# Optimization experiments

Hardware: AMD Instinct MI355X
Metric: run time of the kernel (lower is better)

The kernel has to match this reference:

```python
import jax, jax.numpy as jnp
import numpy as np

N = 50000      # nodes
E = 800000     # edges
P = 3          # pos_dim
F = 64         # feats_dim
M = 32         # m_dim
L = 2          # n_layers
EIN = 2 * F + 1  # edge_input_dim = 129
EPS = 1e-8


def _xavier(key, shape):
    # per-layer stacked xavier-normal weights, shape = (in, out)
    fan_in, fan_out = shape
    std = (2.0 / (fan_in + fan_out)) ** 0.5
    return std * jax.random.normal(key, (L,) + shape, jnp.float32)


def setup_inputs() -> dict:
    key = jax.random.key(0)
    ks = jax.random.split(key, 10)
    x = jax.random.normal(ks[0], (N, P + F), jnp.float32)
    edge_index = jax.random.randint(ks[1], (2, E), 0, N)
    return {
        "x": x,
        "edge_index": edge_index,
        # edge_mlp: Linear(EIN, 2*EIN) -> SiLU -> Linear(2*EIN, M) -> SiLU
        "eW1": _xavier(ks[2], (EIN, 2 * EIN)), "eb1": jnp.zeros((L, 2 * EIN), jnp.float32),
        "eW2": _xavier(ks[3], (2 * EIN, M)),   "eb2": jnp.zeros((L, M), jnp.float32),
        # coors_mlp: Linear(M, 4*M) -> SiLU -> Linear(4*M, 1) -> Tanh
        "cW1": _xavier(ks[4], (M, 4 * M)),     "cb1": jnp.zeros((L, 4 * M), jnp.float32),
        "cW2": _xavier(ks[5], (4 * M, 1)),     "cb2": jnp.zeros((L, 1), jnp.float32),
        # node_mlp: Linear(F+M, 2*F) -> SiLU -> Linear(2*F, F)
        "nW1": _xavier(ks[6], (F + M, 2 * F)), "nb1": jnp.zeros((L, 2 * F), jnp.float32),
        "nW2": _xavier(ks[7], (2 * F, F)),     "nb2": jnp.zeros((L, F), jnp.float32),
        # CoorsNorm learned scale (init 0.01) per layer
        "cscale": jnp.full((L, 1), 0.01, jnp.float32),
    }


def reference(x, edge_index, eW1, eb1, eW2, eb2, cW1, cb1, cW2, cb2,
              nW1, nb1, nW2, nb2, cscale):
    src = edge_index[0]  # x_j (source)
    dst = edge_index[1]  # x_i (target / aggregation index)
    for l in range(L):
        coors, feats = x[:, :P], x[:, P:]
        rel = coors[src] - coors[dst]                       # (E, 3)
        rel_dist = jnp.sum(rel * rel, axis=-1, keepdims=True)  # (E, 1)
        # per-edge message MLP
        e_in = jnp.concatenate([feats[dst], feats[src], rel_dist], axis=-1)  # (E, 129)
        h = jax.nn.silu(e_in @ eW1[l] + eb1[l])             # (E, 258)
        m_ij = jax.nn.silu(h @ eW2[l] + eb2[l])             # (E, 32)
        # coordinate weights: SiLU MLP -> tanh
        cw = jnp.tanh(jax.nn.silu(m_ij @ cW1[l] + cb1[l]) @ cW2[l] + cb2[l])  # (E, 1)
        # CoorsNorm on rel_coors
        norm = jnp.linalg.norm(rel, axis=-1, keepdims=True)
        rel_n = rel / jnp.maximum(norm, EPS) * cscale[l]
        # scatter-aggregate (aggr='add')
        mhat_i = jax.ops.segment_sum(cw * rel_n, dst, num_segments=N)  # (N, 3)
        coors_out = coors + mhat_i
        m_i = jax.ops.segment_sum(m_ij, dst, num_segments=N)           # (N, 32)
        # node update MLP with residual
        n_in = jnp.concatenate([feats, m_i], axis=-1)                  # (N, 96)
        upd = jax.nn.silu(n_in @ nW1[l] + nb1[l]) @ nW2[l] + nb2[l]    # (N, 64)
        x = jnp.concatenate([coors_out, feats + upd], axis=-1)
    return x
```

## Files before the change

kernel.cpp:

```cpp
#include <hip/hip_runtime.h>

#define N_NODES 50000
#define N_EDGES 800000
#define PDIM 3
#define FDIM 64
#define MDIM 32
#define NLAYERS 2
#define EINDIM 129
#define H1 258
#define CH 128
#define NH 128
#define XDIM 67
#define H1T 288
#define HSTR3 104
#define W1T_K 136
#define MLSTR 40
#define NINS 104
#define NH1S 136
#define NW2K 128

typedef __attribute__((ext_vector_type(8))) short short8;
typedef __attribute__((ext_vector_type(4))) float f32x4;

#define LOG2E 1.4426950408889634f

__device__ __forceinline__ float fsilu(float x) {
  float e = __builtin_amdgcn_exp2f(-x * LOG2E);
  return x * __builtin_amdgcn_rcpf(1.0f + e);
}

__device__ __forceinline__ float ftanh(float x) {
  float xc = fminf(fmaxf(x, -15.0f), 15.0f);
  float E = __builtin_amdgcn_exp2f(2.0f * LOG2E * xc);
  return (E - 1.0f) * __builtin_amdgcn_rcpf(E + 1.0f);
}

__device__ __forceinline__ unsigned short f2bf(float f) {
  union { float f; unsigned u; } v; v.f = f;
  unsigned r = v.u + 0x7FFF + ((v.u >> 16) & 1);
  return (unsigned short)(r >> 16);
}

__device__ __forceinline__ unsigned cvt_pk(float lo, float hi) {
  unsigned r;
  asm("v_cvt_pk_bf16_f32 %0, %1, %2" : "=v"(r) : "v"(lo), "v"(hi));
  return r;
}

__device__ __forceinline__ int xcd_swz(int bid, int nwg) {
  const int nx = 8;
  int q = nwg / nx, r = nwg % nx;
  int xcd = bid % nx, idx = bid / nx;
  return (xcd < r) ? xcd * (q + 1) + idx : r * (q + 1) + (xcd - r) * q + idx;
}

#define COUNT_BLOCKS 3125
#define PREP_TOTAL (NLAYERS * (H1T * W1T_K + MDIM * H1T + CH * MDIM + 2 * H1T \
                               + NH * NINS + FDIM * NW2K))
#define PREP_BLOCKS ((PREP_TOTAL + 255) / 256)
#define CONV_BLOCKS ((N_NODES * 8 + 255) / 256)

__global__ void setup_kernel(const int* __restrict__ ei, int* __restrict__ cnt,
                             const float* __restrict__ eW1, const float* __restrict__ eW2,
                             const float* __restrict__ cW1, const float* __restrict__ eb1,
                             const float* __restrict__ nW1, const float* __restrict__ nW2,
                             unsigned short* __restrict__ w1t, unsigned short* __restrict__ w2t,
                             unsigned short* __restrict__ cw1t,
                             unsigned short* __restrict__ nw1t, unsigned short* __restrict__ nw2t,
                             float* __restrict__ b1p, float* __restrict__ wrp,
                             const float* __restrict__ X, unsigned short* __restrict__ Xb) {
  const int bid = blockIdx.x;
  const int tid = threadIdx.x;
  if (bid < COUNT_BLOCKS) {
    int e = bid * 256 + tid;
    if (e < N_EDGES) atomicAdd(&cnt[ei[N_EDGES + e]], 1);
    return;
  }
  if (bid < COUNT_BLOCKS + PREP_BLOCKS) {
    int idx = (bid - COUNT_BLOCKS) * 256 + tid;
    const int n1 = NLAYERS * H1T * W1T_K;
    const int n2 = NLAYERS * MDIM * H1T;
    const int n3 = NLAYERS * CH * MDIM;
    const int n4 = NLAYERS * H1T;
    const int n5 = NLAYERS * NH * NINS;
    const int n6 = NLAYERS * FDIM * NW2K;
    if (idx < n1) {
      int k = idx % W1T_K;
      int rest = idx / W1T_K;
      int j = rest % H1T;
      int l = rest / H1T;
      float v = (k < 128 && j < H1) ? eW1[(l * EINDIM + k) * H1 + j] : 0.0f;
      w1t[idx] = f2bf(v);
    } else if (idx < n1 + n2) {
      int t = idx - n1;
      int k = t % H1T;
      int rest = t / H1T;
      int n = rest % MDIM;
      int l = rest / MDIM;
      float v = (k < H1) ? eW2[(l * H1 + k) * MDIM + n] : 0.0f;
      w2t[t] = f2bf(v);
    } else if (idx < n1 + n2 + n3) {
      int t = idx - n1 - n2;
      int k = t % MDIM;
      int rest = t / MDIM;
      int n = rest % CH;
      int l = rest / CH;
      cw1t[t] = f2bf(cW1[(l * MDIM + k) * CH + n]);
    } else if (idx < n1 + n2 + n3 + n4) {
      int t = idx - n1 - n2 - n3;
      int j = t % H1T;
      int l = t / H1T;
      b1p[t] = (j < H1) ? eb1[l * H1 + j] : 0.0f;
    } else if (idx < n1 + n2 + n3 + 2 * n4) {
      int t = idx - n1 - n2 - n3 - n4;
      int j = t % H1T;
      int l = t / H1T;
      wrp[t] = (j < H1) ? eW1[((size_t)l * EINDIM + 128) * H1 + j] : 0.0f;
    } else if (idx < n1 + n2 + n3 + 2 * n4 + n5) {
      int t = idx - n1 - n2 - n3 - 2 * n4;
      int k = t % NINS;
      int rest = t / NINS;
      int j = rest % NH;
      int l = rest / NH;
      float v = (k < FDIM + MDIM) ? nW1[(l * (FDIM + MDIM) + k) * NH + j] : 0.0f;
      nw1t[t] = f2bf(v);
    } else if (idx < n1 + n2 + n3 + 2 * n4 + n5 + n6) {
      int t = idx - n1 - n2 - n3 - 2 * n4 - n5;
      int k = t % NW2K;
      int rest = t / NW2K;
      int j = rest % FDIM;
      int l = rest / FDIM;
      nw2t[t] = f2bf(nW2[(l * NH + k) * FDIM + j]);
    }
    return;
  }
  {
    int idx = (bid - COUNT_BLOCKS - PREP_BLOCKS) * 256 + tid;
    if (idx >= N_NODES * 8) return;
    int n = idx >> 3, c = idx & 7;
    const float* src = X + n * XDIM + PDIM + c * 8;
    short8 v;
    #pragma unroll
    for (int i = 0; i < 8; ++i) v[i] = (short)f2bf(src[i]);
    *(short8*)&Xb[n * 64 + c * 8] = v;
  }
}

__global__ __launch_bounds__(1024)
void scan_kernel(const int* __restrict__ cnt, int* __restrict__ csr, int* __restrict__ cursor) {
  __shared__ int partial[1024];
  const int tid = threadIdx.x;
  const int CHUNK = 49;
  int base = tid * CHUNK;
  int s = 0;
  for (int i = 0; i < CHUNK; ++i) {
    int idx = base + i;
    if (idx < N_NODES) s += cnt[idx];
  }
  partial[tid] = s;
  __syncthreads();
  for (int off = 1; off < 1024; off <<= 1) {
    int v = (tid >= off) ? partial[tid - off] : 0;
    __syncthreads();
    partial[tid] += v;
    __syncthreads();
  }
  int run = partial[tid] - s;
  for (int i = 0; i < CHUNK; ++i) {
    int idx = base + i;
    if (idx < N_NODES) {
      csr[idx] = run;
      cursor[idx] = run;
      run += cnt[idx];
    }
  }
  if (tid == 1023) csr[N_NODES] = run;
}

__global__ void rank_kernel(const int* __restrict__ ei, int* __restrict__ cursor,
                            int* __restrict__ srcS, int* __restrict__ dstS) {
  int e = blockIdx.x * 256 + threadIdx.x;
  if (e < N_EDGES) {
    int s = ei[e];
    int d = ei[N_EDGES + e];
    int p = atomicAdd(&cursor[d], 1);
    srcS[p] = s;
    dstS[p] = d;
  }
}

__global__ __launch_bounds__(256, 4)
void edge_mfma_kernel(const float* __restrict__ X,
                      const unsigned short* __restrict__ Xb,
                      const int* __restrict__ srcS, const int* __restrict__ dstS,
                      const unsigned short* __restrict__ w1t,
                      const float* __restrict__ b1p, const float* __restrict__ wrp,
                      const unsigned short* __restrict__ w2t, const float* __restrict__ eb2,
                      const unsigned short* __restrict__ cw1t, const float* __restrict__ cb1,
                      const float* __restrict__ cW2, const float* __restrict__ cb2,
                      const float* __restrict__ cscale,
                      unsigned short* __restrict__ ms, float* __restrict__ mh4,
                      int layer)
{
  __shared__ unsigned short hLds[128 * HSTR3];
  __shared__ unsigned short ml[128 * MLSTR];

  const int tid = threadIdx.x;
  const int lane = tid & 63;
  const int wid = tid >> 6;
  const int ln15 = lane & 15;
  const int kg = lane >> 4;
  const int e0 = xcd_swz(blockIdx.x, gridDim.x) * 128;
  const int ew0 = e0 + wid * 32;

  const int eA = ew0 + ln15;
  const int eB = ew0 + 16 + ln15;
  const int sA = srcS[eA], dA = dstS[eA];
  const int sB = srcS[eB], dB = dstS[eB];
  float rxA = X[sA * XDIM + 0] - X[dA * XDIM + 0];
  float ryA = X[sA * XDIM + 1] - X[dA * XDIM + 1];
  float rzA = X[sA * XDIM + 2] - X[dA * XDIM + 2];
  float rxB = X[sB * XDIM + 0] - X[dB * XDIM + 0];
  float ryB = X[sB * XDIM + 1] - X[dB * XDIM + 1];
  float rzB = X[sB * XDIM + 2] - X[dB * XDIM + 2];
  const float distA = rxA * rxA + ryA * ryA + rzA * rzA;
  const float distB = rxB * rxB + ryB * ryB + rzB * rzB;

  short8 einB[2][4];
  #pragma unroll
  for (int ks = 0; ks < 4; ++ks) {
    int nA = (ks < 2) ? dA : sA;
    int nB = (ks < 2) ? dB : sB;
    einB[0][ks] = *(const short8*)&Xb[nA * 64 + (ks & 1) * 32 + kg * 8];
    einB[1][ks] = *(const short8*)&Xb[nB * 64 + (ks & 1) * 32 + kg * 8];
  }

  const unsigned short* W1T = w1t + layer * H1T * W1T_K;
  const float* B1P = b1p + layer * H1T;
  const float* WRP = wrp + layer * H1T;
  const unsigned short* W2T = w2t + layer * MDIM * H1T;
  const float* B2 = eb2 + layer * MDIM;

  float b20 = B2[ln15], b21 = B2[16 + ln15];
  f32x4 mac[2][2];
  #pragma unroll
  for (int et = 0; et < 2; ++et) {
    mac[et][0] = (f32x4){b20, b20, b20, b20};
    mac[et][1] = (f32x4){b21, b21, b21, b21};
  }

  #pragma unroll 1
  for (int chunk = 0; chunk < 3; ++chunk) {
    const int jt0 = chunk * 6;
    #pragma unroll 2
    for (int jl = 0; jl < 6; ++jl) {
      const int jt = jt0 + jl;
      f32x4 b4 = *(const f32x4*)&B1P[jt * 16 + kg * 4];
      f32x4 w4 = *(const f32x4*)&WRP[jt * 16 + kg * 4];
      short8 a[4];
      #pragma unroll
      for (int ks = 0; ks < 4; ++ks)
        a[ks] = *(const short8*)&W1T[(jt * 16 + ln15) * W1T_K + ks * 32 + kg * 8];
      #pragma unroll
      for (int et = 0; et < 2; ++et) {
        const float dv = et ? distB : distA;
        f32x4 acc;
        #pragma unroll
        for (int r = 0; r < 4; ++r) acc[r] = fmaf(dv, w4[r], b4[r]);
        #pragma unroll
        for (int ks = 0; ks < 4; ++ks)
          acc = __builtin_amdgcn_mfma_f32_16x16x32_bf16(a[ks], einB[et][ks], acc, 0, 0, 0);
        uint2 uu;
        uu.x = cvt_pk(fsilu(acc[0]), fsilu(acc[1]));
        uu.y = cvt_pk(fsilu(acc[2]), fsilu(acc[3]));
        *(uint2*)&hLds[(wid * 32 + et * 16 + ln15) * HSTR3 + jl * 16 + kg * 4] = uu;
      }
    }
    #pragma unroll
    for (int ksl = 0; ksl < 3; ++ksl) {
      const int kglob = chunk * 96 + ksl * 32;
      short8 w0 = *(const short8*)&W2T[ln15 * H1T + kglob + kg * 8];
      short8 w1 = *(const short8*)&W2T[(16 + ln15) * H1T + kglob + kg * 8];
      #pragma unroll
      for (int et = 0; et < 2; ++et) {
        short8 ah = *(const short8*)&hLds[(wid * 32 + et * 16 + ln15) * HSTR3 + ksl * 32 + kg * 8];
        mac[et][0] = __builtin_amdgcn_mfma_f32_16x16x32_bf16(ah, w0, mac[et][0], 0, 0, 0);
        mac[et][1] = __builtin_amdgcn_mfma_f32_16x16x32_bf16(ah, w1, mac[et][1], 0, 0, 0);
      }
    }
  }

  #pragma unroll
  for (int et = 0; et < 2; ++et) {
    #pragma unroll
    for (int r = 0; r < 4; ++r) {
      int eg = wid * 32 + et * 16 + kg * 4 + r;
      ml[eg * MLSTR + ln15] = f2bf(fsilu(mac[et][0][r]));
      ml[eg * MLSTR + 16 + ln15] = f2bf(fsilu(mac[et][1][r]));
    }
  }

  const unsigned short* CW1T = cw1t + layer * CH * MDIM;
  const float* CB1 = cb1 + layer * CH;
  const float* CW2v = cW2 + layer * CH;
  short8 amA = *(const short8*)&ml[(wid * 32 + ln15) * MLSTR + kg * 8];
  short8 amB = *(const short8*)&ml[(wid * 32 + 16 + ln15) * MLSTR + kg * 8];
  float psA[4] = {0.f, 0.f, 0.f, 0.f};
  float psB[4] = {0.f, 0.f, 0.f, 0.f};
  #pragma unroll
  for (int nt = 0; nt < 8; ++nt) {
    float cb = CB1[nt * 16 + ln15];
    float w2v = CW2v[nt * 16 + ln15];
    short8 bc = *(const short8*)&CW1T[(nt * 16 + ln15) * MDIM + kg * 8];
    f32x4 cA = {cb, cb, cb, cb};
    f32x4 cB = {cb, cb, cb, cb};
    cA = __builtin_amdgcn_mfma_f32_16x16x32_bf16(amA, bc, cA, 0, 0, 0);
    cB = __builtin_amdgcn_mfma_f32_16x16x32_bf16(amB, bc, cB, 0, 0, 0);
    #pragma unroll
    for (int r = 0; r < 4; ++r) {
      psA[r] += fsilu(cA[r]) * w2v;
      psB[r] += fsilu(cB[r]) * w2v;
    }
  }
  #pragma unroll
  for (int off = 1; off < 16; off <<= 1) {
    #pragma unroll
    for (int r = 0; r < 4; ++r) {
      psA[r] += __shfl_xor(psA[r], off, 64);
      psB[r] += __shfl_xor(psB[r], off, 64);
    }
  }
  float cwvA = 0.0f, cwvB = 0.0f;
  #pragma unroll
  for (int r = 0; r < 4; ++r) {
    float tA = __shfl(psA[r], ((lane & 15) >> 2) * 16, 64);
    float tB = __shfl(psB[r], ((lane & 15) >> 2) * 16, 64);
    if ((lane & 3) == r) { cwvA = tA; cwvB = tB; }
  }

  #pragma unroll
  for (int it = 0; it < 2; ++it) {
    int idx = lane + it * 64;
    int el = idx >> 2, seg = idx & 3;
    short8 v = *(const short8*)&ml[(wid * 32 + el) * MLSTR + seg * 8];
    *(short8*)&ms[(size_t)(ew0 + el) * MDIM + seg * 8] = v;
  }
  if (lane < 32) {
    const int hi = lane >> 4;
    float cwv = hi ? cwvB : cwvA;
    float dv = hi ? distB : distA;
    float rx = hi ? rxB : rxA, ry = hi ? ryB : ryA, rz = hi ? rzB : rzA;
    float cw = ftanh(cwv + cb2[layer]);
    float fac = cw * cscale[layer] / fmaxf(sqrtf(dv), 1e-8f);
    *(float4*)&mh4[(size_t)(ew0 + lane) * 4] = make_float4(fac * rx, fac * ry, fac * rz, 0.0f);
  }
}

__global__ __launch_bounds__(256, 5)
void node_mfma_kernel(const float* __restrict__ Xin,
                      const unsigned short* __restrict__ XbIn,
                      const unsigned short* __restrict__ ms,
                      const float* __restrict__ mh4,
                      const int* __restrict__ csr,
                      const unsigned short* __restrict__ nw1t, const float* __restrict__ nb1,
                      const unsigned short* __restrict__ nw2t, const float* __restrict__ nb2,
                      float* __restrict__ Xout, unsigned short* __restrict__ XbOut,
                      int writeXb, int layer)
{
  __shared__ unsigned short ninLds[64 * NINS];
  __shared__ unsigned short h1Lds[64 * NH1S];
  __shared__ int csrLds[65];
  float* outLds = (float*)h1Lds;

  const int tid = threadIdx.x;
  const int lane = tid & 63;
  const int wid = tid >> 6;
  const int ln15 = lane & 15;
  const int kg = lane >> 4;
  const int n0 = xcd_swz(blockIdx.x, gridDim.x) * 64;

  if (tid < 65) {
    int nn = n0 + tid;
    csrLds[tid] = (nn <= N_NODES) ? csr[nn] : 0;
  }
  #pragma unroll
  for (int it = 0; it < 2; ++it) {
    int idx = tid + it * 256;
    int nl = idx >> 3, c = idx & 7;
    int n = n0 + nl;
    uint4 v = make_uint4(0, 0, 0, 0);
    if (n < N_NODES) v = *(const uint4*)&XbIn[n * 64 + c * 8];
    *(uint4*)&ninLds[nl * NINS + c * 8] = v;
  }
  __syncthreads();

  {
    const int nl = tid >> 2, sub = tid & 3;
    const int n = n0 + nl;
    int off = csrLds[nl], end = csrLds[nl + 1];
    if (n >= N_NODES) { off = 0; end = 0; }
    float s0 = 0, s1 = 0, s2 = 0, s3 = 0, s4 = 0, s5 = 0, s6 = 0, s7 = 0;
    for (int r = off; r < end; ++r) {
      uint4 q = *(const uint4*)&ms[(size_t)r * MDIM + sub * 8];
      union { unsigned u; float f; } t;
      t.u = q.x << 16;         s0 += t.f;
      t.u = q.x & 0xFFFF0000u; s1 += t.f;
      t.u = q.y << 16;         s2 += t.f;
      t.u = q.y & 0xFFFF0000u; s3 += t.f;
      t.u = q.z << 16;         s4 += t.f;
      t.u = q.z & 0xFFFF0000u; s5 += t.f;
      t.u = q.w << 16;         s6 += t.f;
      t.u = q.w & 0xFFFF0000u; s7 += t.f;
    }
    uint4 mo;
    mo.x = cvt_pk(s0, s1);
    mo.y = cvt_pk(s2, s3);
    mo.z = cvt_pk(s4, s5);
    mo.w = cvt_pk(s6, s7);
    *(uint4*)&ninLds[nl * NINS + FDIM + sub * 8] = mo;

    float mx = 0, my = 0, mz = 0;
    for (int r = off + sub; r < end; r += 4) {
      float4 q = *(const float4*)&mh4[(size_t)r * 4];
      mx += q.x; my += q.y; mz += q.z;
    }
    mx += __shfl_xor(mx, 1, 64); mx += __shfl_xor(mx, 2, 64);
    my += __shfl_xor(my, 1, 64); my += __shfl_xor(my, 2, 64);
    mz += __shfl_xor(mz, 1, 64); mz += __shfl_xor(mz, 2, 64);
    if (sub == 0 && n < N_NODES) {
      Xout[n * XDIM + 0] = Xin[n * XDIM + 0] + mx;
      Xout[n * XDIM + 1] = Xin[n * XDIM + 1] + my;
      Xout[n * XDIM + 2] = Xin[n * XDIM + 2] + mz;
    }
  }
  __syncthreads();

  const unsigned short* W1 = nw1t + layer * NH * NINS;
  const float* B1 = nb1 + layer * NH;
  for (int jt = wid; jt < 8; jt += 4) {
    f32x4 b4 = *(const f32x4*)&B1[jt * 16 + kg * 4];
    short8 a[3];
    #pragma unroll
    for (int ks = 0; ks < 3; ++ks)
      a[ks] = *(const short8*)&W1[(jt * 16 + ln15) * NINS + ks * 32 + kg * 8];
    #pragma unroll
    for (int et = 0; et < 4; ++et) {
      f32x4 acc = b4;
      #pragma unroll
      for (int ks = 0; ks < 3; ++ks) {
        short8 b = *(const short8*)&ninLds[(et * 16 + ln15) * NINS + ks * 32 + kg * 8];
        acc = __builtin_amdgcn_mfma_f32_16x16x32_bf16(a[ks], b, acc, 0, 0, 0);
      }
      uint2 uu;
      uu.x = cvt_pk(fsilu(acc[0]), fsilu(acc[1]));
      uu.y = cvt_pk(fsilu(acc[2]), fsilu(acc[3]));
      *(uint2*)&h1Lds[(et * 16 + ln15) * NH1S + jt * 16 + kg * 4] = uu;
    }
  }
  __syncthreads();

  const unsigned short* W2 = nw2t + layer * FDIM * NW2K;
  const float* B2 = nb2 + layer * FDIM;
  f32x4 oacc[4];
  {
    int jt = wid;
    f32x4 b4 = *(const f32x4*)&B2[jt * 16 + kg * 4];
    short8 a[4];
    #pragma unroll
    for (int ks = 0; ks < 4; ++ks)
      a[ks] = *(const short8*)&W2[(jt * 16 + ln15) * NW2K + ks * 32 + kg * 8];
    #pragma unroll
    for (int et = 0; et < 4; ++et) {
      f32x4 acc = b4;
      #pragma unroll
      for (int ks = 0; ks < 4; ++ks) {
        short8 b = *(const short8*)&h1Lds[(et * 16 + ln15) * NH1S + ks * 32 + kg * 8];
        acc = __builtin_amdgcn_mfma_f32_16x16x32_bf16(a[ks], b, acc, 0, 0, 0);
      }
      oacc[et] = acc;
    }
  }
  __syncthreads();
  {
    int jt = wid;
    #pragma unroll
    for (int et = 0; et < 4; ++et)
      *(f32x4*)&outLds[(et * 16 + ln15) * 68 + jt * 16 + kg * 4] = oacc[et];
  }
  __syncthreads();

  #pragma unroll
  for (int it = 0; it < 16; ++it) {
    int idx = tid + it * 256;
    int nl = idx >> 6, c = idx & 63;
    int n = n0 + nl;
    if (n < N_NODES) {
      float v = Xin[n * XDIM + PDIM + c] + outLds[nl * 68 + c];
      Xout[n * XDIM + PDIM + c] = v;
      if (writeXb) XbOut[n * 64 + c] = f2bf(v);
    }
  }
}

extern "C" void kernel_launch(void* const* d_in, const int* in_sizes, int n_in,
                              void* d_out, int out_size, void* d_ws, size_t ws_size,
                              hipStream_t stream) {
  const float* x      = (const float*)d_in[0];
  const int*   ei     = (const int*)d_in[1];
  const float* eW1    = (const float*)d_in[2];
  const float* eb1    = (const float*)d_in[3];
  const float* eW2    = (const float*)d_in[4];
  const float* eb2    = (const float*)d_in[5];
  const float* cW1    = (const float*)d_in[6];
  const float* cb1    = (const float*)d_in[7];
  const float* cW2    = (const float*)d_in[8];
  const float* cb2    = (const float*)d_in[9];
  const float* nW1    = (const float*)d_in[10];
  const float* nb1    = (const float*)d_in[11];
  const float* nW2    = (const float*)d_in[12];
  const float* nb2    = (const float*)d_in[13];
  const float* cscale = (const float*)d_in[14];

  float* ws     = (float*)d_ws;
  float* X1     = ws;
  float* mh4    = X1 + N_NODES * XDIM;
  int*   csr    = (int*)(mh4 + (size_t)N_EDGES * 4);
  int*   cursor = csr + N_NODES + 4;
  int*   cnt    = cursor + N_NODES;
  int*   srcS   = cnt + N_NODES;
  int*   dstS   = srcS + N_EDGES;
  unsigned short* w1t  = (unsigned short*)(dstS + N_EDGES);
  unsigned short* w2t  = w1t + NLAYERS * H1T * W1T_K;
  unsigned short* cw1t = w2t + NLAYERS * MDIM * H1T;
  unsigned short* nw1t = cw1t + NLAYERS * CH * MDIM;
  unsigned short* nw2t = nw1t + NLAYERS * NH * NINS;
  float* b1p = (float*)(nw2t + NLAYERS * FDIM * NW2K);
  float* wrp = b1p + NLAYERS * H1T;
  unsigned short* Xb = (unsigned short*)(wrp + NLAYERS * H1T);
  unsigned short* ms = Xb + (size_t)N_NODES * 64;

  hipMemsetAsync(cnt, 0, N_NODES * sizeof(int), stream);
  setup_kernel<<<COUNT_BLOCKS + PREP_BLOCKS + CONV_BLOCKS, 256, 0, stream>>>(
      ei, cnt, eW1, eW2, cW1, eb1, nW1, nW2,
      w1t, w2t, cw1t, nw1t, nw2t, b1p, wrp, x, Xb);
  scan_kernel<<<1, 1024, 0, stream>>>(cnt, csr, cursor);
  rank_kernel<<<(N_EDGES + 255) / 256, 256, 0, stream>>>(ei, cursor, srcS, dstS);

  const int nodeBlocks = (N_NODES + 63) / 64;
  for (int l = 0; l < NLAYERS; ++l) {
    const float* Xin = (l == 0) ? x : X1;
    float* Xout = (l == 0) ? X1 : (float*)d_out;
    edge_mfma_kernel<<<N_EDGES / 128, 256, 0, stream>>>(
        Xin, Xb, srcS, dstS, w1t, b1p, wrp, w2t, eb2, cw1t, cb1, cW2, cb2, cscale,
        ms, mh4, l);
    node_mfma_kernel<<<nodeBlocks, 256, 0, stream>>>(
        Xin, Xb, ms, mh4, csr, nw1t, nb1, nw2t, nb2, Xout, Xb, (l == 0) ? 1 : 0, l);
  }
}
```

Measured before the change: 661.5 us.

## Shrink edge-kernel hidden staging buffer and split node gather across more lanes

The edge kernel now computes the 258-wide hidden layer in 9 chunks of 32 columns instead of 3 chunks of 96. It feeds each chunk straight into the second MFMA GEMM, which shrinks the per-block LDS staging buffer. The launch-bounds occupancy hint rises from 4 to 6 blocks per CU to exploit the smaller LDS and register footprint. The node kernel's segment-sum gather uses 8 lanes per node over two passes, splitting edges between two lane halves and combining them with shuffles, so each CSR segment loop is shorter. The trade-offs are more loop iterations with less MFMA/LDS overlap in the edge kernel, possible register pressure or spills from the tighter launch bound, and extra shuffles in the node kernel.

```diff
diff --git a/kernel.cpp b/kernel.cpp
--- a/kernel.cpp
+++ b/kernel.cpp
@@ -12,7 +12,7 @@
 #define NH 128
 #define XDIM 67
 #define H1T 288
-#define HSTR3 104
+#define HSTR2 40
 #define W1T_K 136
 #define MLSTR 40
 #define NINS 104
@@ -189,7 +189,7 @@
   }
 }
 
-__global__ __launch_bounds__(256, 4)
+__global__ __launch_bounds__(256, 6)
 void edge_mfma_kernel(const float* __restrict__ X,
                       const unsigned short* __restrict__ Xb,
                       const int* __restrict__ srcS, const int* __restrict__ dstS,
@@ -202,7 +202,7 @@
                       unsigned short* __restrict__ ms, float* __restrict__ mh4,
                       int layer)
 {
-  __shared__ unsigned short hLds[128 * HSTR3];
+  __shared__ unsigned short hLds[128 * HSTR2];
   __shared__ unsigned short ml[128 * MLSTR];
 
   const int tid = threadIdx.x;
@@ -250,11 +250,10 @@
   }
 
   #pragma unroll 1
-  for (int chunk = 0; chunk < 3; ++chunk) {
-    const int jt0 = chunk * 6;
-    #pragma unroll 2
-    for (int jl = 0; jl < 6; ++jl) {
-      const int jt = jt0 + jl;
+  for (int chunk = 0; chunk < 9; ++chunk) {
+    #pragma unroll
+    for (int jl = 0; jl < 2; ++jl) {
+      const int jt = chunk * 2 + jl;
       f32x4 b4 = *(const f32x4*)&B1P[jt * 16 + kg * 4];
       f32x4 w4 = *(const f32x4*)&WRP[jt * 16 + kg * 4];
       short8 a[4];
@@ -273,17 +272,16 @@
         uint2 uu;
         uu.x = cvt_pk(fsilu(acc[0]), fsilu(acc[1]));
         uu.y = cvt_pk(fsilu(acc[2]), fsilu(acc[3]));
-        *(uint2*)&hLds[(wid * 32 + et * 16 + ln15) * HSTR3 + jl * 16 + kg * 4] = uu;
+        *(uint2*)&hLds[(wid * 32 + et * 16 + ln15) * HSTR2 + jl * 16 + kg * 4] = uu;
       }
     }
-    #pragma unroll
-    for (int ksl = 0; ksl < 3; ++ksl) {
-      const int kglob = chunk * 96 + ksl * 32;
+    {
+      const int kglob = chunk * 32;
       short8 w0 = *(const short8*)&W2T[ln15 * H1T + kglob + kg * 8];
       short8 w1 = *(const short8*)&W2T[(16 + ln15) * H1T + kglob + kg * 8];
       #pragma unroll
       for (int et = 0; et < 2; ++et) {
-        short8 ah = *(const short8*)&hLds[(wid * 32 + et * 16 + ln15) * HSTR3 + ksl * 32 + kg * 8];
+        short8 ah = *(const short8*)&hLds[(wid * 32 + et * 16 + ln15) * HSTR2 + kg * 8];
         mac[et][0] = __builtin_amdgcn_mfma_f32_16x16x32_bf16(ah, w0, mac[et][0], 0, 0, 0);
         mac[et][1] = __builtin_amdgcn_mfma_f32_16x16x32_bf16(ah, w1, mac[et][1], 0, 0, 0);
       }
@@ -394,14 +392,18 @@
   }
   __syncthreads();
 
-  {
-    const int nl = tid >> 2, sub = tid & 3;
+  #pragma unroll 1
+  for (int pass = 0; pass < 2; ++pass) {
+    const int nl = (tid >> 3) + pass * 32;
+    const int sub = tid & 7;
+    const int colq = sub & 3;
+    const int rhalf = sub >> 2;
     const int n = n0 + nl;
     int off = csrLds[nl], end = csrLds[nl + 1];
     if (n >= N_NODES) { off = 0; end = 0; }
     float s0 = 0, s1 = 0, s2 = 0, s3 = 0, s4 = 0, s5 = 0, s6 = 0, s7 = 0;
-    for (int r = off; r < end; ++r) {
-      uint4 q = *(const uint4*)&ms[(size_t)r * MDIM + sub * 8];
+    for (int r = off + rhalf; r < end; r += 2) {
+      uint4 q = *(const uint4*)&ms[(size_t)r * MDIM + colq * 8];
       union { unsigned u; float f; } t;
       t.u = q.x << 16;         s0 += t.f;
       t.u = q.x & 0xFFFF0000u; s1 += t.f;
@@ -412,21 +414,30 @@
       t.u = q.w << 16;         s6 += t.f;
       t.u = q.w & 0xFFFF0000u; s7 += t.f;
     }
-    uint4 mo;
-    mo.x = cvt_pk(s0, s1);
-    mo.y = cvt_pk(s2, s3);
-    mo.z = cvt_pk(s4, s5);
-    mo.w = cvt_pk(s6, s7);
-    *(uint4*)&ninLds[nl * NINS + FDIM + sub * 8] = mo;
-
+    s0 += __shfl_xor(s0, 4, 64);
+    s1 += __shfl_xor(s1, 4, 64);
+    s2 += __shfl_xor(s2, 4, 64);
+    s3 += __shfl_xor(s3, 4, 64);
+    s4 += __shfl_xor(s4, 4, 64);
+    s5 += __shfl_xor(s5, 4, 64);
+    s6 += __shfl_xor(s6, 4, 64);
+    s7 += __shfl_xor(s7, 4, 64);
+    if (rhalf == 0) {
+      uint4 mo;
+      mo.x = cvt_pk(s0, s1);
+      mo.y = cvt_pk(s2, s3);
+      mo.z = cvt_pk(s4, s5);
+      mo.w = cvt_pk(s6, s7);
+      *(uint4*)&ninLds[nl * NINS + FDIM + colq * 8] = mo;
+    }
     float mx = 0, my = 0, mz = 0;
-    for (int r = off + sub; r < end; r += 4) {
+    for (int r = off + sub; r < end; r += 8) {
       float4 q = *(const float4*)&mh4[(size_t)r * 4];
       mx += q.x; my += q.y; mz += q.z;
     }
-    mx += __shfl_xor(mx, 1, 64); mx += __shfl_xor(mx, 2, 64);
-    my += __shfl_xor(my, 1, 64); my += __shfl_xor(my, 2, 64);
-    mz += __shfl_xor(mz, 1, 64); mz += __shfl_xor(mz, 2, 64);
+    mx += __shfl_xor(mx, 1, 64); mx += __shfl_xor(mx, 2, 64); mx += __shfl_xor(mx, 4, 64);
+    my += __shfl_xor(my, 1, 64); my += __shfl_xor(my, 2, 64); my += __shfl_xor(my, 4, 64);
+    mz += __shfl_xor(mz, 1, 64); mz += __shfl_xor(mz, 2, 64); mz += __shfl_xor(mz, 4, 64);
     if (sub == 0 && n < N_NODES) {
       Xout[n * XDIM + 0] = Xin[n * XDIM + 0] + mx;
       Xout[n * XDIM + 1] = Xin[n * XDIM + 1] + my;
```

Measured after the change: 1.057 ms. +59.8%, slower.
